# Optimization experiments

Hardware: AMD Instinct MI355X
Metric: run time of the kernel (lower is better)

## Reference

```python
import jax, jax.numpy as jnp
import numpy as np

N_HEADS = 4
HEAD_DIM = 128
FMAP_H, FMAP_W = 32, 32
IN_DIM = 512
BATCH = 16


def setup_inputs() -> dict:
    key = jax.random.key(0)
    k1, k2, k3, k4 = jax.random.split(key, 4)
    scale = HEAD_DIM ** (-0.5)
    x = jax.random.normal(k1, (BATCH, IN_DIM, FMAP_H, FMAP_W), dtype=jnp.float32)
    # 1x1 conv weight producing q,k,v stacked along output channels
    conv_w = jax.random.normal(k2, (3 * N_HEADS * HEAD_DIM, IN_DIM), dtype=jnp.float32) * (IN_DIM ** -0.5)
    pos_h = jax.random.normal(k3, (FMAP_H, HEAD_DIM), dtype=jnp.float32) * scale
    pos_w = jax.random.normal(k4, (FMAP_W, HEAD_DIM), dtype=jnp.float32) * scale
    return {"x": x, "conv_w": conv_w, "pos_h": pos_h, "pos_w": pos_w}


def reference(x, conv_w, pos_h, pos_w):
    B, C, H, W = x.shape
    hw = H * W
    scale = HEAD_DIM ** (-0.5)
    # 1x1 conv == pointwise linear over channels
    qkv = jnp.einsum('bchw,oc->bohw', x, conv_w)               # [B, 3*nh*hd, H, W]
    qkv = qkv.reshape(B, 3, N_HEADS, HEAD_DIM, hw)             # chunk + per-head split
    q = jnp.swapaxes(qkv[:, 0], -1, -2) * scale                # [B, nh, hw, hd]
    k = jnp.swapaxes(qkv[:, 1], -1, -2)
    v = jnp.swapaxes(qkv[:, 2], -1, -2)
    # absolute positional embedding: h[i,:]+w[j,:] flattened over positions
    emb = (pos_h[:, None, :] + pos_w[None, :, :]).reshape(hw, HEAD_DIM)
    sim = jnp.einsum('bhid,bhjd->bhij', q, k) + jnp.einsum('bhid,jd->bhij', q, emb)
    attn = jax.nn.softmax(sim, axis=-1)
    out = jnp.einsum('bhij,bhjd->bhid', attn, v)               # [B, nh, hw, hd]
    out = jnp.swapaxes(out, -1, -2)                            # [B, nh, hd, hw]
    return out.reshape(B, N_HEADS * HEAD_DIM, hw // N_HEADS, N_HEADS)
```

## Files before the change

### kernel.cpp

```cpp
#include <hip/hip_runtime.h>

#define NB 16
#define NH 4
#define HD 128
#define HW 1024
#define CIN 512

typedef short s16x8 __attribute__((ext_vector_type(8)));
typedef short s16x4 __attribute__((ext_vector_type(4)));
typedef float f32x4 __attribute__((ext_vector_type(4)));

static __device__ __forceinline__ short f2bf(float f) {
    union { float f; unsigned u; } v; v.f = f;
    unsigned r = v.u + 0x7fffu + ((v.u >> 16) & 1u);
    return (short)(r >> 16);
}

static __device__ __forceinline__ void gload16(const short* g, short* l) {
    __builtin_amdgcn_global_load_lds(
        (const __attribute__((address_space(1))) unsigned int*)g,
        (__attribute__((address_space(3))) unsigned int*)l, 16, 0, 0);
}

__global__ __launch_bounds__(256) void prep_xw(
    const float* __restrict__ x, const float* __restrict__ w,
    short* __restrict__ xT, short* __restrict__ Wb)
{
    int blk = blockIdx.x;
    if (blk < NB * 16 * 32) {
        int b = blk >> 9, rem = blk & 511;
        int ct = rem >> 5, pt = rem & 31;
        __shared__ float tile[32][33];
        int tc = threadIdx.x >> 5;
        int tp = threadIdx.x & 31;
        const float* xb = x + ((size_t)b * CIN + ct * 32) * HW + pt * 32;
        #pragma unroll
        for (int i = 0; i < 4; i++)
            tile[tc + i * 8][tp] = xb[(size_t)(tc + i * 8) * HW + tp];
        __syncthreads();
        int p = threadIdx.x >> 3, cq = threadIdx.x & 7;
        short* xo = xT + ((size_t)b * HW + pt * 32 + p) * CIN + ct * 32 + cq * 4;
        s16x4 o4 = { f2bf(tile[cq * 4 + 0][p]), f2bf(tile[cq * 4 + 1][p]),
                     f2bf(tile[cq * 4 + 2][p]), f2bf(tile[cq * 4 + 3][p]) };
        *reinterpret_cast<s16x4*>(xo) = o4;
    } else {
        int wb = blk - NB * 16 * 32;
        size_t base = (size_t)wb * 1024 + threadIdx.x * 4;
        const float4 v = *reinterpret_cast<const float4*>(w + base);
        s16x4 o4 = { f2bf(v.x), f2bf(v.y), f2bf(v.z), f2bf(v.w) };
        *reinterpret_cast<s16x4*>(Wb + base) = o4;
    }
}

__global__ __launch_bounds__(256, 3) void qkv_proj(
    const short* __restrict__ xT, const short* __restrict__ Wb,
    const float* __restrict__ pos_h, const float* __restrict__ pos_w,
    short* __restrict__ Q, short* __restrict__ Kp, short* __restrict__ Vt)
{
    __shared__ __align__(1024) char smem[34816];
    short* As = (short*)smem;
    short* Bs = As + 128 * 64;
    short* vb = (short*)smem;

    const int pt = blockIdx.x, ot = blockIdx.y, b = blockIdx.z;
    const int tid = threadIdx.x;
    const int wave = tid >> 6, lane = tid & 63;
    const int l16 = lane & 15, quad = lane >> 4;
    const int wm = (wave & 1) * 64, wn = (wave >> 1) * 64;
    const int o0 = ot * 128, p0 = pt * 128;

    const short* xb = xT + (size_t)b * HW * CIN;

    const int r8 = lane >> 3, c8 = lane & 7;
    const int sch = c8 ^ r8;
    const short* wsrc = Wb + (size_t)(o0 + wave * 32 + r8) * CIN + sch * 8;
    const short* xsrc = xb + (size_t)(p0 + wave * 32 + r8) * CIN + sch * 8;
    short* adst = As + wave * 2048;
    short* bdst = Bs + wave * 2048;

    f32x4 acc[4][4];
    #pragma unroll
    for (int i = 0; i < 4; i++)
        #pragma unroll
        for (int j = 0; j < 4; j++)
            acc[i][j] = f32x4{0.f, 0.f, 0.f, 0.f};

    #pragma unroll 1
    for (int kc = 0; kc < CIN; kc += 64) {
        #pragma unroll
        for (int j = 0; j < 4; j++) {
            gload16(wsrc + kc + (size_t)(j * 8) * CIN, adst + j * 512);
            gload16(xsrc + kc + (size_t)(j * 8) * CIN, bdst + j * 512);
        }
        __syncthreads();
        #pragma unroll
        for (int kk = 0; kk < 2; kk++) {
            s16x8 aF[4], bF[4];
            #pragma unroll
            for (int mi = 0; mi < 4; mi++)
                aF[mi] = *(const s16x8*)(As + (wm + mi * 16 + l16) * 64
                                         + (((kk * 4 + quad) ^ (l16 & 7)) * 8));
            #pragma unroll
            for (int ni = 0; ni < 4; ni++)
                bF[ni] = *(const s16x8*)(Bs + (wn + ni * 16 + l16) * 64
                                         + (((kk * 4 + quad) ^ (l16 & 7)) * 8));
            #pragma unroll
            for (int mi = 0; mi < 4; mi++)
                #pragma unroll
                for (int ni = 0; ni < 4; ni++)
                    acc[mi][ni] = __builtin_amdgcn_mfma_f32_16x16x32_bf16(
                        aF[mi], bF[ni], acc[mi][ni], 0, 0, 0);
        }
        __syncthreads();
    }

    const int s = ot >> 2, h = ot & 3;
    const size_t bh = (size_t)(b * NH + h);

    if (s == 0) {
        const float qs = 0.08838834764831845f * 1.4426950408889634f;
        short* Qb = Q + bh * (size_t)(HW * HD);
        #pragma unroll
        for (int mi = 0; mi < 4; mi++) {
            int d0 = wm + mi * 16 + quad * 4;
            #pragma unroll
            for (int ni = 0; ni < 4; ni++) {
                int p = p0 + wn + ni * 16 + l16;
                f32x4 a = acc[mi][ni];
                s16x4 o4 = { f2bf(a.x * qs), f2bf(a.y * qs),
                             f2bf(a.z * qs), f2bf(a.w * qs) };
                *reinterpret_cast<s16x4*>(Qb + (size_t)p * HD + d0) = o4;
            }
        }
    } else if (s == 1) {
        short* Kb = Kp + bh * (size_t)(HW * HD);
        #pragma unroll
        for (int mi = 0; mi < 4; mi++) {
            int d0 = wm + mi * 16 + quad * 4;
            #pragma unroll
            for (int ni = 0; ni < 4; ni++) {
                int p = p0 + wn + ni * 16 + l16;
                const float4 eh = *reinterpret_cast<const float4*>(pos_h + (p >> 5) * HD + d0);
                const float4 ew = *reinterpret_cast<const float4*>(pos_w + (p & 31) * HD + d0);
                f32x4 a = acc[mi][ni];
                s16x4 o4 = { f2bf(a.x + eh.x + ew.x), f2bf(a.y + eh.y + ew.y),
                             f2bf(a.z + eh.z + ew.z), f2bf(a.w + eh.w + ew.w) };
                *reinterpret_cast<s16x4*>(Kb + (size_t)p * HD + d0) = o4;
            }
        }
    } else {
        __syncthreads();
        #pragma unroll
        for (int mi = 0; mi < 4; mi++) {
            int d0 = wm + mi * 16 + quad * 4;
            #pragma unroll
            for (int ni = 0; ni < 4; ni++) {
                int p = wn + ni * 16 + l16;
                f32x4 a = acc[mi][ni];
                vb[(d0 + 0) * 136 + p] = f2bf(a.x);
                vb[(d0 + 1) * 136 + p] = f2bf(a.y);
                vb[(d0 + 2) * 136 + p] = f2bf(a.z);
                vb[(d0 + 3) * 136 + p] = f2bf(a.w);
            }
        }
        __syncthreads();
        short* Vb = Vt + bh * (size_t)(HD * HW);
        int d = tid >> 1, half = tid & 1;
        #pragma unroll
        for (int j = 0; j < 8; j++) {
            const short* row = vb + d * 136;
            int base = (half * 2 + (j >> 2)) * 32 + (j & 3) * 4;
            s16x4 lo = *(const s16x4*)(row + base);
            s16x4 hi = *(const s16x4*)(row + base + 16);
            s16x8 v8 = { lo[0], lo[1], lo[2], lo[3],
                         hi[0], hi[1], hi[2], hi[3] };
            *reinterpret_cast<s16x8*>(Vb + (size_t)d * HW + p0 + half * 64 + j * 8) = v8;
        }
    }
}

__global__ __launch_bounds__(256, 2) void attn_fused(
    const short* __restrict__ Q, const short* __restrict__ Kp,
    const short* __restrict__ Vt, float* __restrict__ out)
{
    __shared__ __align__(1024) short Ks[2][64 * 128];
    __shared__ __align__(1024) short Vs[2][128 * 64];

    const int flat = blockIdx.x;
    const int qt = flat >> 6;
    const int bh = flat & 63;
    const int tid = threadIdx.x;
    const int wave = tid >> 6, lane = tid & 63;
    const int l16 = lane & 15, quad = lane >> 4;

    const short* Qb = Q + (size_t)bh * (HW * HD);
    const short* Kb = Kp + (size_t)bh * (HW * HD);
    const short* Vb = Vt + (size_t)bh * (HD * HW);

    const int q0 = qt * 128 + wave * 32;

    s16x8 bQ[2][4];
    #pragma unroll
    for (int nt = 0; nt < 2; nt++)
        #pragma unroll
        for (int kk = 0; kk < 4; kk++)
            bQ[nt][kk] = *(const s16x8*)(Qb + (size_t)(q0 + nt * 16 + l16) * HD
                                         + kk * 32 + quad * 8);

    s16x8 ones;
    #pragma unroll
    for (int j = 0; j < 8; j++) ones[j] = (short)0x3F80;

    f32x4 Oacc[2][8];
    #pragma unroll
    for (int mt = 0; mt < 2; mt++)
        #pragma unroll
        for (int dt = 0; dt < 8; dt++)
            Oacc[mt][dt] = f32x4{0.f, 0.f, 0.f, 0.f};
    f32x4 lacc[2] = { f32x4{0.f, 0.f, 0.f, 0.f}, f32x4{0.f, 0.f, 0.f, 0.f} };

    const int kRow = lane >> 4;
    const int vRow = lane >> 3;
    const int vSch = (lane & 7) ^ vRow;

    #define STAGE(buf, tile)                                                  \
        do {                                                                  \
            _Pragma("unroll")                                                 \
            for (int j = 0; j < 4; j++) {                                     \
                int kkey = wave * 16 + j * 4 + kRow;                          \
                gload16(Kb + ((size_t)((tile) * 64 + kkey)) * HD              \
                           + (((lane & 15) ^ (j * 4 + kRow)) * 8),            \
                        &Ks[buf][(wave * 16 + j * 4) * 128] + lane * 8);      \
                int vd = wave * 32 + j * 8 + vRow;                            \
                gload16(Vb + (size_t)vd * HW + (tile) * 64 + vSch * 8,        \
                        &Vs[buf][(wave * 32 + j * 8) * 64] + lane * 8);       \
            }                                                                 \
        } while (0)

    STAGE(0, 0);
    __syncthreads();

    #pragma unroll 1
    for (int kt = 0; kt < 16; kt++) {
        const int cur = kt & 1, nxt = cur ^ 1;
        const short* ks = Ks[cur];
        const short* vs = Vs[cur];

        STAGE(nxt, (kt + 1) & 15);

        f32x4 c[4][2];
        __builtin_amdgcn_s_setprio(1);
        #pragma unroll
        for (int mtp = 0; mtp < 4; mtp++) {
            s16x8 aK[4];
            #pragma unroll
            for (int kk = 0; kk < 4; kk++)
                aK[kk] = *(const s16x8*)(ks + (mtp * 16 + l16) * 128
                                         + (((kk * 4 + quad) ^ l16) * 8));
            c[mtp][0] = f32x4{0.f, 0.f, 0.f, 0.f};
            c[mtp][1] = f32x4{0.f, 0.f, 0.f, 0.f};
            #pragma unroll
            for (int kk = 0; kk < 4; kk++) {
                c[mtp][0] = __builtin_amdgcn_mfma_f32_16x16x32_bf16(
                    aK[kk], bQ[0][kk], c[mtp][0], 0, 0, 0);
                c[mtp][1] = __builtin_amdgcn_mfma_f32_16x16x32_bf16(
                    aK[kk], bQ[1][kk], c[mtp][1], 0, 0, 0);
            }
        }
        __builtin_amdgcn_s_setprio(0);

        s16x8 bV[2][8];
        #pragma unroll
        for (int h2 = 0; h2 < 2; h2++)
            #pragma unroll
            for (int dt = 0; dt < 8; dt++)
                bV[h2][dt] = *(const s16x8*)(vs + (dt * 16 + l16) * 64
                                             + (((h2 * 4 + quad) ^ (l16 & 7)) * 8));

        #pragma unroll
        for (int h = 0; h < 2; h++) {
            s16x8 aP[2];
            #pragma unroll
            for (int mt = 0; mt < 2; mt++) {
                f32x4 e0 = c[2 * h][mt], e1 = c[2 * h + 1][mt];
                aP[mt] = s16x8{
                    f2bf(__builtin_amdgcn_exp2f(e0[0])),
                    f2bf(__builtin_amdgcn_exp2f(e0[1])),
                    f2bf(__builtin_amdgcn_exp2f(e0[2])),
                    f2bf(__builtin_amdgcn_exp2f(e0[3])),
                    f2bf(__builtin_amdgcn_exp2f(e1[0])),
                    f2bf(__builtin_amdgcn_exp2f(e1[1])),
                    f2bf(__builtin_amdgcn_exp2f(e1[2])),
                    f2bf(__builtin_amdgcn_exp2f(e1[3])) };
            }

            __builtin_amdgcn_s_setprio(1);
            #pragma unroll
            for (int mt = 0; mt < 2; mt++)
                lacc[mt] = __builtin_amdgcn_mfma_f32_16x16x32_bf16(
                    aP[mt], ones, lacc[mt], 0, 0, 0);

            #pragma unroll
            for (int dt = 0; dt < 8; dt++) {
                #pragma unroll
                for (int mt = 0; mt < 2; mt++)
                    Oacc[mt][dt] = __builtin_amdgcn_mfma_f32_16x16x32_bf16(
                        aP[mt], bV[h][dt], Oacc[mt][dt], 0, 0, 0);
            }
            __builtin_amdgcn_s_setprio(0);
        }
        __syncthreads();
    }
    #undef STAGE

    float* ob = out + (size_t)bh * (HD * HW);
    #pragma unroll
    for (int mt = 0; mt < 2; mt++) {
        float inv[4];
        #pragma unroll
        for (int r = 0; r < 4; r++) inv[r] = __builtin_amdgcn_rcpf(lacc[mt][r]);
        int prow = q0 + mt * 16 + quad * 4;
        #pragma unroll
        for (int dt = 0; dt < 8; dt++) {
            int d = dt * 16 + l16;
            f32x4 o = Oacc[mt][dt];
            float4 o4 = { o[0] * inv[0], o[1] * inv[1],
                          o[2] * inv[2], o[3] * inv[3] };
            *reinterpret_cast<float4*>(ob + (size_t)d * HW + prow) = o4;
        }
    }
}

extern "C" void kernel_launch(void* const* d_in, const int* in_sizes, int n_in,
                              void* d_out, int out_size, void* d_ws, size_t ws_size,
                              hipStream_t stream) {
    const float* x  = (const float*)d_in[0];
    const float* w  = (const float*)d_in[1];
    const float* ph = (const float*)d_in[2];
    const float* pw = (const float*)d_in[3];

    const size_t BHPD = (size_t)NB * NH * HW * HD;
    short* Q    = (short*)d_ws;
    short* Kp   = Q + BHPD;
    short* Vt   = Kp + BHPD;
    short* xT   = Vt + BHPD;
    short* Wb   = xT + (size_t)NB * HW * CIN;
    float* outp = (float*)d_out;

    prep_xw<<<dim3(NB * 16 * 32 + 768), 256, 0, stream>>>(x, w, xT, Wb);
    qkv_proj<<<dim3(8, 12, NB), 256, 0, stream>>>(xT, Wb, ph, pw, Q, Kp, Vt);
    attn_fused<<<dim3(512), 256, 0, stream>>>(Q, Kp, Vt, outp);
}
```

Measured before the change: 164.7 us.

## Load K and V fragments directly from global memory, dropping LDS staging

The double-buffered LDS staging of K and V tiles, together with its per-iteration barrier, is removed. Each wave now reads its MFMA operand fragments straight from global memory into registers. This eliminates LDS traffic and block-wide synchronisation, but the four waves now each fetch the same K/V data separately, relying on the L1/L2 caches, and global latency is no longer hidden by the async prefetch. Register pressure also grows because aK is held as a full 4x4 array.

```diff
diff --git a/kernel.cpp b/kernel.cpp
--- a/kernel.cpp
+++ b/kernel.cpp
@@ -183,9 +183,6 @@
     const short* __restrict__ Q, const short* __restrict__ Kp,
     const short* __restrict__ Vt, float* __restrict__ out)
 {
-    __shared__ __align__(1024) short Ks[2][64 * 128];
-    __shared__ __align__(1024) short Vs[2][128 * 64];
-
     const int flat = blockIdx.x;
     const int qt = flat >> 6;
     const int bh = flat & 63;
@@ -219,52 +216,31 @@
             Oacc[mt][dt] = f32x4{0.f, 0.f, 0.f, 0.f};
     f32x4 lacc[2] = { f32x4{0.f, 0.f, 0.f, 0.f}, f32x4{0.f, 0.f, 0.f, 0.f} };
 
-    const int kRow = lane >> 4;
-    const int vRow = lane >> 3;
-    const int vSch = (lane & 7) ^ vRow;
-
-    #define STAGE(buf, tile)                                                  \
-        do {                                                                  \
-            _Pragma("unroll")                                                 \
-            for (int j = 0; j < 4; j++) {                                     \
-                int kkey = wave * 16 + j * 4 + kRow;                          \
-                gload16(Kb + ((size_t)((tile) * 64 + kkey)) * HD              \
-                           + (((lane & 15) ^ (j * 4 + kRow)) * 8),            \
-                        &Ks[buf][(wave * 16 + j * 4) * 128] + lane * 8);      \
-                int vd = wave * 32 + j * 8 + vRow;                            \
-                gload16(Vb + (size_t)vd * HW + (tile) * 64 + vSch * 8,        \
-                        &Vs[buf][(wave * 32 + j * 8) * 64] + lane * 8);       \
-            }                                                                 \
-        } while (0)
-
-    STAGE(0, 0);
-    __syncthreads();
+    const short* kbase = Kb + l16 * HD + quad * 8;
+    const short* vbase = Vb + (size_t)l16 * HW + quad * 8;
 
     #pragma unroll 1
     for (int kt = 0; kt < 16; kt++) {
-        const int cur = kt & 1, nxt = cur ^ 1;
-        const short* ks = Ks[cur];
-        const short* vs = Vs[cur];
-
-        STAGE(nxt, (kt + 1) & 15);
+        s16x8 aK[4][4];
+        #pragma unroll
+        for (int mtp = 0; mtp < 4; mtp++)
+            #pragma unroll
+            for (int kk = 0; kk < 4; kk++)
+                aK[mtp][kk] = *(const s16x8*)(kbase
+                    + (size_t)(kt * 64 + mtp * 16) * HD + kk * 32);
 
         f32x4 c[4][2];
         __builtin_amdgcn_s_setprio(1);
         #pragma unroll
         for (int mtp = 0; mtp < 4; mtp++) {
-            s16x8 aK[4];
-            #pragma unroll
-            for (int kk = 0; kk < 4; kk++)
-                aK[kk] = *(const s16x8*)(ks + (mtp * 16 + l16) * 128
-                                         + (((kk * 4 + quad) ^ l16) * 8));
             c[mtp][0] = f32x4{0.f, 0.f, 0.f, 0.f};
             c[mtp][1] = f32x4{0.f, 0.f, 0.f, 0.f};
             #pragma unroll
             for (int kk = 0; kk < 4; kk++) {
                 c[mtp][0] = __builtin_amdgcn_mfma_f32_16x16x32_bf16(
-                    aK[kk], bQ[0][kk], c[mtp][0], 0, 0, 0);
+                    aK[mtp][kk], bQ[0][kk], c[mtp][0], 0, 0, 0);
                 c[mtp][1] = __builtin_amdgcn_mfma_f32_16x16x32_bf16(
-                    aK[kk], bQ[1][kk], c[mtp][1], 0, 0, 0);
+                    aK[mtp][kk], bQ[1][kk], c[mtp][1], 0, 0, 0);
             }
         }
         __builtin_amdgcn_s_setprio(0);
@@ -274,8 +250,8 @@
         for (int h2 = 0; h2 < 2; h2++)
             #pragma unroll
             for (int dt = 0; dt < 8; dt++)
-                bV[h2][dt] = *(const s16x8*)(vs + (dt * 16 + l16) * 64
-                                             + (((h2 * 4 + quad) ^ (l16 & 7)) * 8));
+                bV[h2][dt] = *(const s16x8*)(vbase
+                    + (size_t)(dt * 16) * HW + kt * 64 + h2 * 32);
 
         #pragma unroll
         for (int h = 0; h < 2; h++) {
@@ -309,9 +285,7 @@
             }
             __builtin_amdgcn_s_setprio(0);
         }
-        __syncthreads();
-    }
-    #undef STAGE
+    }
 
     float* ob = out + (size_t)bh * (HD * HW);
     #pragma unroll
```

Measured after the change: 254.8 us. +54.7%, slower.
